# Optimization experiments

Hardware: AMD Instinct MI355X
Metric: run time of the kernel (lower is better)

Reference implementation:

```python
import jax, jax.numpy as jnp
import numpy as np

B, N, D = 1024, 7, 1024
SQRT_D = float(np.sqrt(D))
MAX_CTX, MAX_VIB = 0.24, 0.26
VIB_IDX, CTX_IDX = 3, N - 1

ADJ = jnp.asarray(np.array([
    [1, 1, 0, 0, 1, 1, 1],
    [1, 1, 1, 1, 1, 1, 1],
    [0, 1, 1, 0, 1, 0, 1],
    [0, 1, 0, 1, 1, 1, 1],
    [1, 1, 1, 1, 1, 1, 1],
    [1, 1, 0, 1, 1, 1, 1],
    [1, 1, 1, 1, 1, 1, 1]], dtype=np.float32))


def _gelu(x):
    return jax.nn.gelu(x, approximate=False)


def setup_inputs() -> dict:
    key = jax.random.key(0)
    ks = jax.random.split(key, 20)
    s = 0.02
    def w(k, shape):
        return jax.random.normal(k, shape, dtype=jnp.float32) * s
    return {
        "nodes": jax.random.normal(ks[0], (B, N, D), dtype=jnp.float32),
        "Wq": w(ks[1], (D, D)), "bq": jnp.zeros((D,), jnp.float32),
        "Wk": w(ks[2], (D, D)), "bk": jnp.zeros((D,), jnp.float32),
        "Wv": w(ks[3], (D, D)), "bv": jnp.zeros((D,), jnp.float32),
        "We1": w(ks[4], (3 * D, D)), "be1": jnp.zeros((D,), jnp.float32),
        "We2": w(ks[5], (D, 1)), "be2": jnp.zeros((1,), jnp.float32),
        "Wu1": w(ks[6], (2 * D, D)), "bu1": jnp.zeros((D,), jnp.float32),
        "Wu2": w(ks[7], (D, D)), "bu2": jnp.zeros((D,), jnp.float32),
        "Wi1": w(ks[8], (2 * D, D)), "bi1": jnp.zeros((D,), jnp.float32),
        "Wi2": w(ks[9], (D, 1)), "bi2": jnp.zeros((1,), jnp.float32),
    }


def _cap_importance(imp):
    cap = jnp.ones((N,), imp.dtype).at[VIB_IDX].set(MAX_VIB).at[CTX_IDX].set(MAX_CTX)
    free = jnp.ones((N,), imp.dtype).at[VIB_IDX].set(0.0).at[CTX_IDX].set(0.0)[None, :]
    capped = jnp.minimum(imp, cap[None, :])
    free_mass = (imp * free).sum(axis=1, keepdims=True)
    residual = jnp.clip(1.0 - capped.sum(axis=1, keepdims=True), 0.0)
    uniform = free / jnp.maximum(free.sum(axis=1, keepdims=True), 1.0)
    free_share = jnp.where(free_mass > 1e-6,
                           imp * free / jnp.maximum(free_mass, 1e-6),
                           uniform)
    redis = capped + free_share * residual
    return redis / jnp.maximum(redis.sum(axis=1, keepdims=True), 1e-6)


def _physics_loss(upd):
    norms = jnp.linalg.norm(upd, axis=-1)  # [B,N]
    dots = jnp.einsum('bnd,bmd->bnm', upd, upd)
    cos = dots / jnp.maximum(norms[:, :, None] * norms[:, None, :], 1e-8)
    eye = jnp.eye(N, dtype=upd.dtype)
    edge_loss = ((1.0 - cos) * ADJ[None]).sum() / jnp.maximum(ADJ.sum() * upd.shape[0], 1.0) * upd.shape[0]
    # note: torch sums over batch too -> divide by ADJ.sum() only
    edge_loss = ((1.0 - cos) * ADJ[None]).sum() / jnp.maximum(ADJ.sum(), 1.0)
    non_mask = (1.0 - ADJ) * (1.0 - eye)
    non_loss = (jax.nn.relu(cos - 0.35) * non_mask[None]).sum() / jnp.maximum(non_mask.sum(), 1.0)
    return edge_loss + 0.5 * non_loss


def _alignment_loss(upd, fused):
    fn = fused / jnp.maximum(jnp.linalg.norm(fused, axis=-1, keepdims=True), 1e-12)
    nn_ = upd / jnp.maximum(jnp.linalg.norm(upd, axis=-1, keepdims=True), 1e-12)
    cos = jnp.einsum('bnd,bd->bn', nn_, fn)
    return (1.0 - cos).mean()


def reference(nodes, Wq, bq, Wk, bk, Wv, bv, We1, be1, We2, be2,
              Wu1, bu1, Wu2, bu2, Wi1, bi1, Wi2, bi2):
    q = nodes @ Wq + bq
    k = nodes @ Wk + bk
    v = nodes @ Wv + bv
    logits = jnp.einsum('bnd,bmd->bnm', q, k) / SQRT_D
    # edge gate: cat([left, right, ctx]) @ We1 == left@Wa + right@Wb + ctx@Wc
    Wa, Wb, Wc = We1[:D], We1[D:2 * D], We1[2 * D:]
    la = nodes @ Wa                      # [B,N,D] (left varies over axis n)
    rb = nodes @ Wb                      # [B,N,D] (right varies over axis m)
    cc = nodes[:, -1] @ Wc               # [B,D]   (ctx broadcast)
    h = la[:, :, None, :] + rb[:, None, :, :] + cc[:, None, None, :] + be1
    edge_logits = (_gelu(h) @ We2 + be2)[..., 0]  # [B,N,N]
    masked = logits + edge_logits + (ADJ[None] - 1.0) * 10000.0
    attn = jax.nn.softmax(masked, axis=-1)
    messages = jnp.einsum('bnm,bmd->bnd', attn, v)
    upd_in = jnp.concatenate([nodes, messages], axis=-1)
    updated = _gelu(upd_in @ Wu1 + bu1) @ Wu2 + bu2 + nodes
    gq = jnp.broadcast_to(updated[:, -1:, :], updated.shape)
    imp_in = jnp.concatenate([updated, gq], axis=-1)
    imp_logits = (_gelu(imp_in @ Wi1 + bi1) @ Wi2 + bi2)[..., 0]
    imp = jax.nn.softmax(imp_logits, axis=-1)
    imp = _cap_importance(imp)
    fused = jnp.einsum('bn,bnd->bd', imp, updated)
    phys = _physics_loss(updated)
    align = _alignment_loss(updated, fused)
    return (fused, updated, imp, attn, phys + align * 0.0, align)
```

## Files before the change

kernel.cpp:

```cpp
#include <hip/hip_runtime.h>
#include <hip/hip_bf16.h>


typedef __attribute__((ext_vector_type(8))) short bf16x8;
typedef __attribute__((ext_vector_type(4))) float f32x4;

__constant__ float c_adj[49] = {
    1,1,0,0,1,1,1,
    1,1,1,1,1,1,1,
    0,1,1,0,1,0,1,
    0,1,0,1,1,1,1,
    1,1,1,1,1,1,1,
    1,1,0,1,1,1,1,
    1,1,1,1,1,1,1};

__device__ __forceinline__ float gelu_f(float x) {
    return 0.5f * x * (1.0f + erff(x * 0.7071067811865476f));
}
__device__ __forceinline__ float b2f(unsigned short u) {
    unsigned int x = ((unsigned int)u) << 16;
    union { unsigned int i; float f; } c; c.i = x; return c.f;
}
__device__ __forceinline__ unsigned short f2b(float f) {
    __hip_bfloat16 h = __float2bfloat16(f);
    union { __hip_bfloat16 b; unsigned short u; } c; c.b = h; return c.u;
}

__device__ __forceinline__ void gload_lds16(const void* g, void* l) {
    __builtin_amdgcn_global_load_lds(
        (const __attribute__((address_space(1))) unsigned int*)g,
        (__attribute__((address_space(3))) unsigned int*)l, 16, 0, 0);
}

__device__ __forceinline__ int maprow(int r, int mode) {
    if (mode == 1) return r * 7 + 6;
    if (mode == 2) return r - r % 7 + 6;
    return r;
}

__global__ __launch_bounds__(256) void gemm128(
    const unsigned short* __restrict__ A1, int a1Mode,
    const unsigned short* __restrict__ A2, int a2Mode,
    const unsigned short* __restrict__ WT, int ldw,
    const float* __restrict__ bias,
    const float* __restrict__ resid,
    float* __restrict__ Cf,
    unsigned short* __restrict__ Cb, size_t segStride,
    int K, int act)
{
    __shared__ short As[128 * 32];
    __shared__ short Bs[128 * 32];
    const int tid = threadIdx.x;
    const int lane = tid & 63;
    const int w = tid >> 6;
    const int wr = (w >> 1) * 64;
    const int wc = (w & 1) * 64;
    const int row0 = blockIdx.y * 128;
    const int col0 = blockIdx.x * 128;
    const int fr = lane & 15;
    const int fko = (((lane >> 4) ^ ((fr >> 1) & 3)) << 3);

    f32x4 acc[4][4] = {};

    for (int k0 = 0; k0 < K; k0 += 32) {
        const unsigned short* srcA; int mode; int kbase;
        if (k0 < 1024) { srcA = A1; mode = a1Mode; kbase = k0; }
        else           { srcA = A2; mode = a2Mode; kbase = k0 - 1024; }
        #pragma unroll
        for (int rnd = 0; rnd < 2; ++rnd) {
            int c = rnd * 256 + tid;
            int m = c >> 2, ch = c & 3;
            int kc = (ch ^ ((m >> 1) & 3)) * 8;
            int rr = maprow(row0 + m, mode);
            gload_lds16(srcA + (size_t)rr * 1024 + kbase + kc, &As[c * 8]);
        }
        #pragma unroll
        for (int rnd = 0; rnd < 2; ++rnd) {
            int c = rnd * 256 + tid;
            int n = c >> 2, ch = c & 3;
            int kc = (ch ^ ((n >> 1) & 3)) * 8;
            gload_lds16(WT + (size_t)(col0 + n) * ldw + k0 + kc, &Bs[c * 8]);
        }
        __syncthreads();
        bf16x8 af[4], bf_[4];
        #pragma unroll
        for (int i = 0; i < 4; ++i)
            af[i] = *(const bf16x8*)(&As[(wr + i * 16 + fr) * 32 + fko]);
        #pragma unroll
        for (int j = 0; j < 4; ++j)
            bf_[j] = *(const bf16x8*)(&Bs[(wc + j * 16 + fr) * 32 + fko]);
        #pragma unroll
        for (int i = 0; i < 4; ++i)
            #pragma unroll
            for (int j = 0; j < 4; ++j)
                acc[i][j] = __builtin_amdgcn_mfma_f32_16x16x32_bf16(
                    af[i], bf_[j], acc[i][j], 0, 0, 0);
        __syncthreads();
    }

    const int qrow = (lane >> 4) * 4;
    const int qcol = lane & 15;
    #pragma unroll
    for (int i = 0; i < 4; ++i) {
        int rbase = row0 + wr + i * 16 + qrow;
        #pragma unroll
        for (int j = 0; j < 4; ++j) {
            int c = col0 + wc + j * 16 + qcol;
            float bv = bias ? bias[c] : 0.0f;
            int seg = c >> 10, c0 = c & 1023;
            #pragma unroll
            for (int reg = 0; reg < 4; ++reg) {
                int r = rbase + reg;
                float vv = acc[i][j][reg] + bv;
                if (act) vv = gelu_f(vv);
                if (resid) vv += resid[(size_t)r * 1024 + c];
                if (Cf) Cf[(size_t)r * 1024 + c] = vv;
                if (Cb) Cb[(size_t)seg * segStride + (size_t)r * 1024 + c0] = f2b(vv);
            }
        }
    }
}

__global__ __launch_bounds__(256) void gemm64x128(
    const unsigned short* __restrict__ A1, int a1Mode,
    const unsigned short* __restrict__ A2, int a2Mode,
    const unsigned short* __restrict__ WT, int ldw,
    const float* __restrict__ bias,
    const float* __restrict__ resid,
    float* __restrict__ Cf,
    unsigned short* __restrict__ Cb,
    int K, int act)
{
    __shared__ short As[64 * 32];
    __shared__ short Bs[128 * 32];
    const int tid = threadIdx.x;
    const int lane = tid & 63;
    const int w = tid >> 6;
    const int wc = w * 32;
    const int row0 = blockIdx.y * 64;
    const int col0 = blockIdx.x * 128;
    const int fr = lane & 15;
    const int fko = (((lane >> 4) ^ ((fr >> 1) & 3)) << 3);

    f32x4 acc[4][2] = {};

    for (int k0 = 0; k0 < K; k0 += 32) {
        const unsigned short* srcA; int mode; int kbase;
        if (k0 < 1024) { srcA = A1; mode = a1Mode; kbase = k0; }
        else           { srcA = A2; mode = a2Mode; kbase = k0 - 1024; }
        {
            int m = tid >> 2, ch = tid & 3;
            int kc = (ch ^ ((m >> 1) & 3)) * 8;
            int rr = maprow(row0 + m, mode);
            gload_lds16(srcA + (size_t)rr * 1024 + kbase + kc, &As[tid * 8]);
        }
        #pragma unroll
        for (int rnd = 0; rnd < 2; ++rnd) {
            int c = rnd * 256 + tid;
            int n = c >> 2, ch = c & 3;
            int kc = (ch ^ ((n >> 1) & 3)) * 8;
            gload_lds16(WT + (size_t)(col0 + n) * ldw + k0 + kc, &Bs[c * 8]);
        }
        __syncthreads();
        bf16x8 af[4], bf_[2];
        #pragma unroll
        for (int i = 0; i < 4; ++i)
            af[i] = *(const bf16x8*)(&As[(i * 16 + fr) * 32 + fko]);
        #pragma unroll
        for (int j = 0; j < 2; ++j)
            bf_[j] = *(const bf16x8*)(&Bs[(wc + j * 16 + fr) * 32 + fko]);
        #pragma unroll
        for (int i = 0; i < 4; ++i)
            #pragma unroll
            for (int j = 0; j < 2; ++j)
                acc[i][j] = __builtin_amdgcn_mfma_f32_16x16x32_bf16(
                    af[i], bf_[j], acc[i][j], 0, 0, 0);
        __syncthreads();
    }

    const int qrow = (lane >> 4) * 4;
    const int qcol = lane & 15;
    #pragma unroll
    for (int i = 0; i < 4; ++i) {
        int rbase = row0 + i * 16 + qrow;
        #pragma unroll
        for (int j = 0; j < 2; ++j) {
            int c = col0 + wc + j * 16 + qcol;
            float bv = bias ? bias[c] : 0.0f;
            #pragma unroll
            for (int reg = 0; reg < 4; ++reg) {
                int r = rbase + reg;
                float vv = acc[i][j][reg] + bv;
                if (act) vv = gelu_f(vv);
                if (resid) vv += resid[(size_t)r * 1024 + c];
                if (Cf) Cf[(size_t)r * 1024 + c] = vv;
                if (Cb) Cb[(size_t)r * 1024 + c] = f2b(vv);
            }
        }
    }
}

__global__ __launch_bounds__(256) void cast_f2b(
    const float* __restrict__ in, unsigned short* __restrict__ out, int n)
{
    int i = (blockIdx.x * 256 + threadIdx.x) * 4;
    if (i >= n) return;
    float4 v = *(const float4*)(in + i);
    ushort4 o;
    o.x = f2b(v.x); o.y = f2b(v.y); o.z = f2b(v.z); o.w = f2b(v.w);
    *(ushort4*)(out + i) = o;
}

__global__ __launch_bounds__(256) void tcast_all(
    const float* __restrict__ Wq, const float* __restrict__ Wk,
    const float* __restrict__ Wv, const float* __restrict__ We1,
    const float* __restrict__ Wu1, const float* __restrict__ Wu2,
    const float* __restrict__ Wi1,
    unsigned short* __restrict__ WT_all, unsigned short* __restrict__ Wu1T,
    unsigned short* __restrict__ Wu2T, unsigned short* __restrict__ Wi1T)
{
    const int z = blockIdx.z;
    const float* src; unsigned short* dst; int R;
    switch (z) {
        case 0: src = Wq;            dst = WT_all;               R = 1024; break;
        case 1: src = Wk;            dst = WT_all + 1024 * 1024; R = 1024; break;
        case 2: src = Wv;            dst = WT_all + 2048 * 1024; R = 1024; break;
        case 3: src = We1;           dst = WT_all + 3072 * 1024; R = 1024; break;
        case 4: src = We1 + 1048576; dst = WT_all + 4096 * 1024; R = 1024; break;
        case 5: src = We1 + 2097152; dst = WT_all + 5120 * 1024; R = 1024; break;
        case 6: src = Wu1;           dst = Wu1T;                 R = 2048; break;
        case 7: src = Wu2;           dst = Wu2T;                 R = 1024; break;
        default: src = Wi1;          dst = Wi1T;                 R = 2048; break;
    }
    const int rt = blockIdx.y * 32;
    if (rt >= R) return;
    const int ct = blockIdx.x * 32;
    __shared__ float t[32][33];
    const int tx = threadIdx.x & 31, ty = threadIdx.x >> 5;
    #pragma unroll
    for (int s = 0; s < 4; ++s)
        t[ty + s * 8][tx] = src[(size_t)(rt + ty + s * 8) * 1024 + ct + tx];
    __syncthreads();
    #pragma unroll
    for (int s = 0; s < 4; ++s)
        dst[(size_t)(ct + ty + s * 8) * R + rt + tx] = f2b(t[tx][ty + s * 8]);
}

__global__ void build_bias(const float* __restrict__ bq,
                           const float* __restrict__ bk,
                           const float* __restrict__ bv,
                           float* __restrict__ bias_all)
{
    int i = blockIdx.x * 256 + threadIdx.x;
    if (i >= 5120) return;
    int seg = i >> 10, c = i & 1023;
    float v = 0.f;
    if (seg == 0) v = bq[c];
    else if (seg == 1) v = bk[c];
    else if (seg == 2) v = bv[c];
    bias_all[i] = v;
}

__global__ __launch_bounds__(256) void attn_msg_b(
    const unsigned short* __restrict__ q, const unsigned short* __restrict__ k,
    const unsigned short* __restrict__ v,
    const unsigned short* __restrict__ la, const unsigned short* __restrict__ rb,
    const float* __restrict__ cc,
    const float* __restrict__ We2, const float* __restrict__ be2,
    float* __restrict__ attn_out, unsigned short* __restrict__ msg)
{
    const int bn = blockIdx.x;
    const int b = bn / 7, n = bn % 7;
    const int tid = threadIdx.x;
    const int lane = tid & 63, wv = tid >> 6;
    const int d0 = tid * 4;
    __shared__ float red[8];
    __shared__ float sm[7];

    float qv[4], lav[4], ccv[4], wev[4];
    {
        ushort4 q4 = *(const ushort4*)(q + (size_t)bn * 1024 + d0);
        ushort4 l4 = *(const ushort4*)(la + (size_t)bn * 1024 + d0);
        float4 c4 = *(const float4*)(cc + (size_t)b * 1024 + d0);
        float4 w4 = *(const float4*)(We2 + d0);
        qv[0] = b2f(q4.x); qv[1] = b2f(q4.y); qv[2] = b2f(q4.z); qv[3] = b2f(q4.w);
        lav[0] = b2f(l4.x); lav[1] = b2f(l4.y); lav[2] = b2f(l4.z); lav[3] = b2f(l4.w);
        ccv[0] = c4.x; ccv[1] = c4.y; ccv[2] = c4.z; ccv[3] = c4.w;
        wev[0] = w4.x; wev[1] = w4.y; wev[2] = w4.z; wev[3] = w4.w;
    }
    for (int m = 0; m < 7; ++m) {
        ushort4 k4 = *(const ushort4*)(k  + (size_t)(b * 7 + m) * 1024 + d0);
        ushort4 r4 = *(const ushort4*)(rb + (size_t)(b * 7 + m) * 1024 + d0);
        float s1 = qv[0] * b2f(k4.x) + qv[1] * b2f(k4.y)
                 + qv[2] * b2f(k4.z) + qv[3] * b2f(k4.w);
        float s2 = gelu_f(lav[0] + b2f(r4.x) + ccv[0]) * wev[0]
                 + gelu_f(lav[1] + b2f(r4.y) + ccv[1]) * wev[1]
                 + gelu_f(lav[2] + b2f(r4.z) + ccv[2]) * wev[2]
                 + gelu_f(lav[3] + b2f(r4.w) + ccv[3]) * wev[3];
        #pragma unroll
        for (int off = 32; off > 0; off >>= 1) {
            s1 += __shfl_down(s1, off);
            s2 += __shfl_down(s2, off);
        }
        if (lane == 0) { red[wv * 2] = s1; red[wv * 2 + 1] = s2; }
        __syncthreads();
        if (tid == 0) {
            float d1 = red[0] + red[2] + red[4] + red[6];
            float d2 = red[1] + red[3] + red[5] + red[7];
            sm[m] = d1 * (1.0f / 32.0f) + d2 + be2[0]
                  + (c_adj[n * 7 + m] - 1.0f) * 10000.0f;
        }
        __syncthreads();
    }
    if (tid == 0) {
        float mx = sm[0];
        #pragma unroll
        for (int m = 1; m < 7; ++m) mx = fmaxf(mx, sm[m]);
        float e[7], s = 0.f;
        #pragma unroll
        for (int m = 0; m < 7; ++m) { e[m] = expf(sm[m] - mx); s += e[m]; }
        float inv = 1.0f / s;
        #pragma unroll
        for (int m = 0; m < 7; ++m) {
            float wgt = e[m] * inv;
            sm[m] = wgt;
            attn_out[(size_t)bn * 7 + m] = wgt;
        }
    }
    __syncthreads();
    float wr_[7];
    #pragma unroll
    for (int m = 0; m < 7; ++m) wr_[m] = sm[m];
    float s0 = 0.f, s1 = 0.f, s2 = 0.f, s3 = 0.f;
    #pragma unroll
    for (int m = 0; m < 7; ++m) {
        ushort4 v4 = *(const ushort4*)(v + (size_t)(b * 7 + m) * 1024 + d0);
        s0 += wr_[m] * b2f(v4.x); s1 += wr_[m] * b2f(v4.y);
        s2 += wr_[m] * b2f(v4.z); s3 += wr_[m] * b2f(v4.w);
    }
    ushort4 o;
    o.x = f2b(s0); o.y = f2b(s1); o.z = f2b(s2); o.w = f2b(s3);
    *(ushort4*)(msg + (size_t)bn * 1024 + d0) = o;
}

__global__ __launch_bounds__(256) void row_dot_b(
    const unsigned short* __restrict__ H, const float* __restrict__ w2,
    const float* __restrict__ b2, float* __restrict__ out)
{
    const int r = blockIdx.x;
    const int tid = threadIdx.x;
    const int lane = tid & 63, wv = tid >> 6;
    __shared__ float red[4];
    const int d0 = tid * 4;
    ushort4 h4 = *(const ushort4*)(H + (size_t)r * 1024 + d0);
    float4 w4 = *(const float4*)(w2 + d0);
    float s = b2f(h4.x) * w4.x + b2f(h4.y) * w4.y
            + b2f(h4.z) * w4.z + b2f(h4.w) * w4.w;
    #pragma unroll
    for (int off = 32; off > 0; off >>= 1) s += __shfl_down(s, off);
    if (lane == 0) red[wv] = s;
    __syncthreads();
    if (tid == 0) out[r] = red[0] + red[1] + red[2] + red[3] + b2[0];
}

__global__ __launch_bounds__(256) void imp_fused_k(
    const float* __restrict__ logits, const float* __restrict__ upd,
    float* __restrict__ imp_out, float* __restrict__ fused_out)
{
    const int b = blockIdx.x;
    const int tid = threadIdx.x;
    __shared__ float w[7];
    if (tid == 0) {
        float l[7], e[7];
        float mx = -1e30f;
        for (int i = 0; i < 7; ++i) { l[i] = logits[b * 7 + i]; mx = fmaxf(mx, l[i]); }
        float s = 0.f;
        for (int i = 0; i < 7; ++i) { e[i] = expf(l[i] - mx); s += e[i]; }
        float inv = 1.0f / s;
        float imp[7];
        for (int i = 0; i < 7; ++i) imp[i] = e[i] * inv;
        const float cap[7] = {1.f, 1.f, 1.f, 0.26f, 1.f, 1.f, 0.24f};
        const float fr[7]  = {1.f, 1.f, 1.f, 0.f,   1.f, 1.f, 0.f};
        float capped[7], capsum = 0.f, fmass = 0.f;
        for (int i = 0; i < 7; ++i) {
            capped[i] = fminf(imp[i], cap[i]);
            capsum += capped[i];
            fmass += imp[i] * fr[i];
        }
        float residual = fmaxf(1.0f - capsum, 0.0f);
        float redis[7], rs = 0.f;
        for (int i = 0; i < 7; ++i) {
            float fs = (fmass > 1e-6f) ? imp[i] * fr[i] / fmaxf(fmass, 1e-6f)
                                       : fr[i] * 0.2f;
            redis[i] = capped[i] + fs * residual;
            rs += redis[i];
        }
        float invr = 1.0f / fmaxf(rs, 1e-6f);
        for (int i = 0; i < 7; ++i) {
            float wi = redis[i] * invr;
            w[i] = wi;
            imp_out[b * 7 + i] = wi;
        }
    }
    __syncthreads();
    float wr[7];
    #pragma unroll
    for (int i = 0; i < 7; ++i) wr[i] = w[i];
    #pragma unroll
    for (int j = 0; j < 4; ++j) {
        int d = tid + j * 256;
        float s = 0.f;
        #pragma unroll
        for (int nn2 = 0; nn2 < 7; ++nn2)
            s += wr[nn2] * upd[(size_t)(b * 7 + nn2) * 1024 + d];
        fused_out[(size_t)b * 1024 + d] = s;
    }
}

__global__ void zero_acc(float* a) { if (threadIdx.x < 4) a[threadIdx.x] = 0.f; }

__global__ __launch_bounds__(256) void physics_k(
    const float* __restrict__ upd, const float* __restrict__ fused,
    float* __restrict__ accums)
{
    const int b = blockIdx.x;
    const int tid = threadIdx.x;
    const int lane = tid & 63, wv = tid >> 6;
    __shared__ float u[7][1024];
    __shared__ float f[1024];
    __shared__ float wred[4][36];
    for (int idx = tid; idx < 7 * 1024; idx += 256)
        u[idx >> 10][idx & 1023] = upd[(size_t)b * 7168 + idx];
    for (int d = tid; d < 1024; d += 256)
        f[d] = fused[(size_t)b * 1024 + d];
    __syncthreads();

    float vals[36];
    #pragma unroll
    for (int i = 0; i < 36; ++i) vals[i] = 0.f;
    for (int d = tid; d < 1024; d += 256) {
        float x[7];
        #pragma unroll
        for (int n = 0; n < 7; ++n) x[n] = u[n][d];
        float fv = f[d];
        int idx = 0;
        #pragma unroll
        for (int n = 0; n < 7; ++n) {
            #pragma unroll
            for (int m = n; m < 7; ++m) vals[idx++] += x[n] * x[m];
        }
        #pragma unroll
        for (int n = 0; n < 7; ++n) vals[28 + n] += x[n] * fv;
        vals[35] += fv * fv;
    }
    #pragma unroll
    for (int i = 0; i < 36; ++i) {
        float s = vals[i];
        #pragma unroll
        for (int off = 32; off > 0; off >>= 1) s += __shfl_down(s, off);
        if (lane == 0) wred[wv][i] = s;
    }
    __syncthreads();
    if (tid == 0) {
        float tv[36];
        for (int i = 0; i < 36; ++i)
            tv[i] = wred[0][i] + wred[1][i] + wred[2][i] + wred[3][i];
        auto didx = [](int n, int m) -> int {
            if (n > m) { int t = n; n = m; m = t; }
            return n * 7 - n * (n - 1) / 2 + (m - n);
        };
        float norms[7];
        for (int n = 0; n < 7; ++n) norms[n] = sqrtf(tv[didx(n, n)]);
        float e = 0.f, nl = 0.f;
        for (int n = 0; n < 7; ++n)
            for (int m = 0; m < 7; ++m) {
                float cos_ = tv[didx(n, m)] / fmaxf(norms[n] * norms[m], 1e-8f);
                float adj = c_adj[n * 7 + m];
                e += (1.0f - cos_) * adj;
                if (adj == 0.0f && n != m) nl += fmaxf(cos_ - 0.35f, 0.0f);
            }
        float fnorm = sqrtf(tv[35]);
        float al = 0.f;
        for (int n = 0; n < 7; ++n) {
            float cosn = tv[28 + n] /
                         (fmaxf(norms[n], 1e-12f) * fmaxf(fnorm, 1e-12f));
            al += 1.0f - cosn;
        }
        atomicAdd(&accums[0], e);
        atomicAdd(&accums[1], nl);
        atomicAdd(&accums[2], al);
    }
}

__global__ void finalize_k(const float* __restrict__ a,
                           float* __restrict__ phys_o,
                           float* __restrict__ align_o)
{
    phys_o[0]  = a[0] / 41.0f + 0.5f * (a[1] / 8.0f);
    align_o[0] = a[2] * (1.0f / 7168.0f);
}

extern "C" void kernel_launch(void* const* d_in, const int* in_sizes, int n_in,
                              void* d_out, int out_size, void* d_ws, size_t ws_size,
                              hipStream_t stream)
{
    const float* nodes = (const float*)d_in[0];
    const float* Wq  = (const float*)d_in[1];
    const float* bq  = (const float*)d_in[2];
    const float* Wk  = (const float*)d_in[3];
    const float* bk  = (const float*)d_in[4];
    const float* Wv  = (const float*)d_in[5];
    const float* bv  = (const float*)d_in[6];
    const float* We1 = (const float*)d_in[7];
    const float* be1 = (const float*)d_in[8];
    const float* We2 = (const float*)d_in[9];
    const float* be2 = (const float*)d_in[10];
    const float* Wu1 = (const float*)d_in[11];
    const float* bu1 = (const float*)d_in[12];
    const float* Wu2 = (const float*)d_in[13];
    const float* bu2 = (const float*)d_in[14];
    const float* Wi1 = (const float*)d_in[15];
    const float* bi1 = (const float*)d_in[16];
    const float* Wi2 = (const float*)d_in[17];
    const float* bi2 = (const float*)d_in[18];

    float* out = (float*)d_out;
    float* fused_o = out;
    float* upd_o   = out + 1048576;
    float* imp_o   = out + 1048576 + 7340032;
    float* attn_o  = imp_o + 7168;
    float* phys_o  = attn_o + 50176;
    float* align_o = phys_o + 1;

    const size_t BIG = 7340032;
    const size_t MEG = 1048576;
    char* p = (char*)d_ws;
    unsigned short* nodes_b = (unsigned short*)p; p += BIG * 2;
    unsigned short* qb      = (unsigned short*)p; p += BIG * 2;
    unsigned short* kb      = (unsigned short*)p; p += BIG * 2;
    unsigned short* vb      = (unsigned short*)p; p += BIG * 2;
    unsigned short* lab     = (unsigned short*)p; p += BIG * 2;
    unsigned short* rbb     = (unsigned short*)p; p += BIG * 2;
    unsigned short* WT_all  = (unsigned short*)p; p += (size_t)6144 * 1024 * 2;
    unsigned short* Wu1T    = (unsigned short*)p; p += 2 * MEG * 2;
    unsigned short* Wu2T    = (unsigned short*)p; p += MEG * 2;
    unsigned short* Wi1T    = (unsigned short*)p; p += 2 * MEG * 2;
    float* bias_all = (float*)p; p += 5120 * 4;
    float* ccf = (float*)p; p += MEG * 4;
    float* il  = (float*)p; p += 7168 * 4;
    float* acc = (float*)p; p += 4 * 4;
    unsigned short* msgb = lab;
    unsigned short* hub  = qb;
    unsigned short* updb = kb;
    unsigned short* hib  = vb;

    dim3 blk(256);

    cast_f2b<<<dim3(7168), blk, 0, stream>>>(nodes, nodes_b, 7340032);
    tcast_all<<<dim3(32, 64, 9), blk, 0, stream>>>(Wq, Wk, Wv, We1, Wu1, Wu2, Wi1,
                                                   WT_all, Wu1T, Wu2T, Wi1T);
    build_bias<<<dim3(20), blk, 0, stream>>>(bq, bk, bv, bias_all);

    gemm128<<<dim3(40, 56), blk, 0, stream>>>(
        nodes_b, 0, nullptr, 0, WT_all, 1024, bias_all, nullptr,
        nullptr, qb, BIG, 1024, 0);

    gemm64x128<<<dim3(8, 16), blk, 0, stream>>>(
        nodes_b, 1, nullptr, 0, WT_all + (size_t)5120 * 1024, 1024, be1, nullptr,
        ccf, nullptr, 1024, 0);

    attn_msg_b<<<dim3(7168), blk, 0, stream>>>(qb, kb, vb, lab, rbb, ccf, We2, be2,
                                               attn_o, msgb);

    gemm128<<<dim3(8, 56), blk, 0, stream>>>(
        nodes_b, 0, msgb, 0, Wu1T, 2048, bu1, nullptr, nullptr, hub, 0, 2048, 1);
    gemm128<<<dim3(8, 56), blk, 0, stream>>>(
        hub, 0, nullptr, 0, Wu2T, 1024, bu2, nodes, upd_o, updb, 0, 1024, 0);
    gemm128<<<dim3(8, 56), blk, 0, stream>>>(
        updb, 0, updb, 2, Wi1T, 2048, bi1, nullptr, nullptr, hib, 0, 2048, 1);

    row_dot_b<<<dim3(7168), blk, 0, stream>>>(hib, Wi2, bi2, il);
    imp_fused_k<<<dim3(1024), blk, 0, stream>>>(il, upd_o, imp_o, fused_o);
    zero_acc<<<1, 64, 0, stream>>>(acc);
    physics_k<<<dim3(1024), blk, 0, stream>>>(upd_o, fused_o, acc);
    finalize_k<<<1, 1, 0, stream>>>(acc, phys_o, align_o);
}
```

Before: 579.1 us.

## Replace fused QKV/edge projection GEMM with 256x256 tiled, 4-stage pipelined kernel

Adds a 512-thread GEMM kernel with 256x256 output tiles, a 4-deep LDS ring buffer fed by direct global-to-LDS loads, XOR-swizzled LDS layout, XCD-aware block remapping and split half-tile MFMA phases with priority hints. It replaces the 128x128 GEMM for the large 7168x5120 projection. The goal is more data reuse per tile and better overlap of loads with MFMA work. The cost is 128 KB of LDS and fewer, larger workgroups (560), which limits occupancy.

Result: slower. 591.8 us (+2.2%).

```diff
diff --git a/kernel.cpp b/kernel.cpp
--- a/kernel.cpp
+++ b/kernel.cpp
@@ -36,6 +36,145 @@
     if (mode == 1) return r * 7 + 6;
     if (mode == 2) return r - r % 7 + 6;
     return r;
+}
+
+__global__ __launch_bounds__(512) void gemm256(
+    const unsigned short* __restrict__ A,
+    const unsigned short* __restrict__ WT, int ldw,
+    const float* __restrict__ bias,
+    unsigned short* __restrict__ Cb, size_t segStride,
+    int K)
+{
+    __shared__ short As[4 * 256 * 32];
+    __shared__ short Bs[4 * 256 * 32];
+
+    const int tid  = threadIdx.x;
+    const int lane = tid & 63;
+    const int w    = tid >> 6;
+    const int wm   = w >> 2;
+    const int wn   = w & 3;
+    const int wmr  = wm * 128;
+    const int wnr  = wn * 64;
+
+    int lin = blockIdx.y * gridDim.x + blockIdx.x;
+    const int nwg = gridDim.x * gridDim.y;
+    const int cpx = nwg >> 3;
+    lin = (lin & 7) * cpx + (lin >> 3);
+    const int row0 = (lin / gridDim.x) * 256;
+    const int col0 = (lin % gridDim.x) * 256;
+
+    const int fr  = lane & 15;
+    const int fko = (((lane >> 4) ^ ((fr >> 1) & 3)) << 3);
+
+    int srow[2], skc[2], ldsoff[2];
+    #pragma unroll
+    for (int ld = 0; ld < 2; ++ld) {
+        int s = ld * 512 + tid;
+        int r = s >> 2, ch = s & 3;
+        srow[ld]   = r;
+        skc[ld]    = (ch ^ ((r >> 1) & 3)) * 8;
+        ldsoff[ld] = s * 8;
+    }
+
+    const int NT = K >> 5;
+
+    f32x4 acc[8][4] = {};
+    bf16x8 af[4], bf_[4];
+
+    #pragma unroll
+    for (int u0 = 0; u0 < 4; ++u0) {
+        int tu = u0 >> 1, slot = tu;
+        #pragma unroll
+        for (int ld = 0; ld < 2; ++ld) {
+            if ((u0 & 1) == 0)
+                gload_lds16(A + (size_t)(row0 + srow[ld]) * K + tu * 32 + skc[ld],
+                            &As[slot * 8192 + ldsoff[ld]]);
+            else
+                gload_lds16(WT + (size_t)(col0 + srow[ld]) * ldw + tu * 32 + skc[ld],
+                            &Bs[slot * 8192 + ldsoff[ld]]);
+        }
+    }
+    asm volatile("s_waitcnt vmcnt(4)" ::: "memory");
+    asm volatile("s_barrier" ::: "memory");
+
+    for (int kt = 0; kt < NT; ++kt) {
+        const short* Ab = &As[(kt & 3) * 8192];
+        const short* Bb = &Bs[(kt & 3) * 8192];
+
+        {
+            #pragma unroll
+            for (int i = 0; i < 4; ++i)
+                af[i] = *(const bf16x8*)(Ab + (wmr + i * 16 + fr) * 32 + fko);
+            #pragma unroll
+            for (int j = 0; j < 4; ++j)
+                bf_[j] = *(const bf16x8*)(Bb + (wnr + j * 16 + fr) * 32 + fko);
+            int u = 2 * kt + 4;
+            if (u < 2 * NT) {
+                int tu = u >> 1, slot = tu & 3;
+                #pragma unroll
+                for (int ld = 0; ld < 2; ++ld)
+                    gload_lds16(A + (size_t)(row0 + srow[ld]) * K + tu * 32 + skc[ld],
+                                &As[slot * 8192 + ldsoff[ld]]);
+            }
+            asm volatile("s_barrier" ::: "memory");
+            asm volatile("s_waitcnt lgkmcnt(0)" ::: "memory");
+            __builtin_amdgcn_s_setprio(1);
+            #pragma unroll
+            for (int i = 0; i < 4; ++i)
+                #pragma unroll
+                for (int j = 0; j < 4; ++j)
+                    acc[i][j] = __builtin_amdgcn_mfma_f32_16x16x32_bf16(
+                        af[i], bf_[j], acc[i][j], 0, 0, 0);
+            __builtin_amdgcn_s_setprio(0);
+            asm volatile("s_barrier" ::: "memory");
+        }
+
+        {
+            #pragma unroll
+            for (int i = 0; i < 4; ++i)
+                af[i] = *(const bf16x8*)(Ab + (wmr + (4 + i) * 16 + fr) * 32 + fko);
+            int u = 2 * kt + 5;
+            if (u < 2 * NT) {
+                int tu = u >> 1, slot = tu & 3;
+                #pragma unroll
+                for (int ld = 0; ld < 2; ++ld)
+                    gload_lds16(WT + (size_t)(col0 + srow[ld]) * ldw + tu * 32 + skc[ld],
+                                &Bs[slot * 8192 + ldsoff[ld]]);
+            }
+            if (kt >= NT - 2) asm volatile("s_waitcnt vmcnt(0)" ::: "memory");
+            else              asm volatile("s_waitcnt vmcnt(4)" ::: "memory");
+            asm volatile("s_barrier" ::: "memory");
+            asm volatile("s_waitcnt lgkmcnt(0)" ::: "memory");
+            __builtin_amdgcn_s_setprio(1);
+            #pragma unroll
+            for (int i = 0; i < 4; ++i)
+                #pragma unroll
+                for (int j = 0; j < 4; ++j)
+                    acc[4 + i][j] = __builtin_amdgcn_mfma_f32_16x16x32_bf16(
+                        af[i], bf_[j], acc[4 + i][j], 0, 0, 0);
+            __builtin_amdgcn_s_setprio(0);
+            asm volatile("s_barrier" ::: "memory");
+        }
+    }
+
+    const int qrow = (lane >> 4) * 4;
+    const int qcol = lane & 15;
+    #pragma unroll
+    for (int mf = 0; mf < 8; ++mf) {
+        int rbase = row0 + wmr + mf * 16 + qrow;
+        #pragma unroll
+        for (int nf = 0; nf < 4; ++nf) {
+            int c = col0 + wnr + nf * 16 + qcol;
+            float bv = bias ? bias[c] : 0.0f;
+            int seg = c >> 10, c0 = c & 1023;
+            #pragma unroll
+            for (int reg = 0; reg < 4; ++reg) {
+                int r = rbase + reg;
+                Cb[(size_t)seg * segStride + (size_t)r * 1024 + c0] =
+                    f2b(acc[mf][nf][reg] + bv);
+            }
+        }
+    }
 }
 
 __global__ __launch_bounds__(256) void gemm128(
@@ -561,9 +700,8 @@
                                                    WT_all, Wu1T, Wu2T, Wi1T);
     build_bias<<<dim3(20), blk, 0, stream>>>(bq, bk, bv, bias_all);
 
-    gemm128<<<dim3(40, 56), blk, 0, stream>>>(
-        nodes_b, 0, nullptr, 0, WT_all, 1024, bias_all, nullptr,
-        nullptr, qb, BIG, 1024, 0);
+    gemm256<<<dim3(20, 28), dim3(512), 0, stream>>>(
+        nodes_b, WT_all, 1024, bias_all, qb, BIG, 1024);
 
     gemm64x128<<<dim3(8, 16), blk, 0, stream>>>(
         nodes_b, 1, nullptr, 0, WT_all + (size_t)5120 * 1024, 1024, be1, nullptr,
```

## Double-buffer LDS in gemm128 with XCD-aware block remap and fold zero kernel

Applied to the files above, without the earlier changes.

The main GEMM now uses two LDS buffers so the next K-tile's global-to-LDS loads are issued before the MFMAs on the current tile, with one waitcnt and barrier per iteration instead of two syncthreads. Workgroup IDs are remapped so consecutive tiles land on the same XCD, which should improve L2 reuse, and MFMA sections run at raised wave priority. The separate zero_acc launch is folded into build_bias. The cost is doubled LDS use, which may lower occupancy, and the remap assumes the grid size divides evenly by 8.

After: 581.4 us. Within noise of the previous version (+0.4%).

```diff
diff --git a/kernel.cpp b/kernel.cpp
--- a/kernel.cpp
+++ b/kernel.cpp
@@ -38,7 +38,7 @@
     return r;
 }
 
-__global__ __launch_bounds__(256) void gemm128(
+__global__ __launch_bounds__(256) void gemm128db(
     const unsigned short* __restrict__ A1, int a1Mode,
     const unsigned short* __restrict__ A2, int a2Mode,
     const unsigned short* __restrict__ WT, int ldw,
@@ -48,54 +48,81 @@
     unsigned short* __restrict__ Cb, size_t segStride,
     int K, int act)
 {
-    __shared__ short As[128 * 32];
-    __shared__ short Bs[128 * 32];
+    __shared__ short As[2][128 * 32];
+    __shared__ short Bs[2][128 * 32];
     const int tid = threadIdx.x;
     const int lane = tid & 63;
     const int w = tid >> 6;
     const int wr = (w >> 1) * 64;
     const int wc = (w & 1) * 64;
-    const int row0 = blockIdx.y * 128;
-    const int col0 = blockIdx.x * 128;
+
+    int lin = blockIdx.y * gridDim.x + blockIdx.x;
+    const int nwg = gridDim.x * gridDim.y;
+    const int cpx = nwg >> 3;
+    lin = (lin & 7) * cpx + (lin >> 3);
+    const int row0 = (lin / gridDim.x) * 128;
+    const int col0 = (lin % gridDim.x) * 128;
+
     const int fr = lane & 15;
     const int fko = (((lane >> 4) ^ ((fr >> 1) & 3)) << 3);
 
-    f32x4 acc[4][4] = {};
-
-    for (int k0 = 0; k0 < K; k0 += 32) {
+    const int NTt = K >> 5;
+
+    auto stage = [&](int ktn) {
+        int k0n = ktn * 32;
         const unsigned short* srcA; int mode; int kbase;
-        if (k0 < 1024) { srcA = A1; mode = a1Mode; kbase = k0; }
-        else           { srcA = A2; mode = a2Mode; kbase = k0 - 1024; }
+        if (k0n < 1024) { srcA = A1; mode = a1Mode; kbase = k0n; }
+        else            { srcA = A2; mode = a2Mode; kbase = k0n - 1024; }
+        short* Adst = &As[ktn & 1][0];
+        short* Bdst = &Bs[ktn & 1][0];
         #pragma unroll
         for (int rnd = 0; rnd < 2; ++rnd) {
             int c = rnd * 256 + tid;
             int m = c >> 2, ch = c & 3;
             int kc = (ch ^ ((m >> 1) & 3)) * 8;
             int rr = maprow(row0 + m, mode);
-            gload_lds16(srcA + (size_t)rr * 1024 + kbase + kc, &As[c * 8]);
+            gload_lds16(srcA + (size_t)rr * 1024 + kbase + kc, Adst + c * 8);
         }
         #pragma unroll
         for (int rnd = 0; rnd < 2; ++rnd) {
             int c = rnd * 256 + tid;
             int n = c >> 2, ch = c & 3;
             int kc = (ch ^ ((n >> 1) & 3)) * 8;
-            gload_lds16(WT + (size_t)(col0 + n) * ldw + k0 + kc, &Bs[c * 8]);
-        }
-        __syncthreads();
-        bf16x8 af[4], bf_[4];
+            gload_lds16(WT + (size_t)(col0 + n) * ldw + k0n + kc, Bdst + c * 8);
+        }
+    };
+
+    f32x4 acc[4][4] = {};
+
+    stage(0);
+    asm volatile("s_waitcnt vmcnt(0)" ::: "memory");
+    asm volatile("s_barrier" ::: "memory");
+
+    for (int kt = 0; kt < NTt; ++kt) {
+        const short* Ab = &As[kt & 1][0];
+        const short* Bb = &Bs[kt & 1][0];
+
+        if (kt + 1 < NTt) stage(kt + 1);
+
+        bf16x8 af[4], bfv[4];
         #pragma unroll
         for (int i = 0; i < 4; ++i)
-            af[i] = *(const bf16x8*)(&As[(wr + i * 16 + fr) * 32 + fko]);
+            af[i] = *(const bf16x8*)(Ab + (wr + i * 16 + fr) * 32 + fko);
         #pragma unroll
         for (int j = 0; j < 4; ++j)
-            bf_[j] = *(const bf16x8*)(&Bs[(wc + j * 16 + fr) * 32 + fko]);
+            bfv[j] = *(const bf16x8*)(Bb + (wc + j * 16 + fr) * 32 + fko);
+
+        __builtin_amdgcn_s_setprio(1);
         #pragma unroll
         for (int i = 0; i < 4; ++i)
             #pragma unroll
             for (int j = 0; j < 4; ++j)
                 acc[i][j] = __builtin_amdgcn_mfma_f32_16x16x32_bf16(
-                    af[i], bf_[j], acc[i][j], 0, 0, 0);
-        __syncthreads();
+                    af[i], bfv[j], acc[i][j], 0, 0, 0);
+        __builtin_amdgcn_s_setprio(0);
+
+        asm volatile("s_waitcnt vmcnt(0)" ::: "memory");
+        asm volatile("s_barrier" ::: "memory");
     }
 
     const int qrow = (lane >> 4) * 4;
@@ -249,9 +276,11 @@
 __global__ void build_bias(const float* __restrict__ bq,
                            const float* __restrict__ bk,
                            const float* __restrict__ bv,
-                           float* __restrict__ bias_all)
+                           float* __restrict__ bias_all,
+                           float* __restrict__ acc)
 {
     int i = blockIdx.x * 256 + threadIdx.x;
+    if (i < 4) acc[i] = 0.f;
     if (i >= 5120) return;
     int seg = i >> 10, c = i & 1023;
     float v = 0.f;
@@ -416,8 +445,6 @@
         fused_out[(size_t)b * 1024 + d] = s;
     }
 }
-
-__global__ void zero_acc(float* a) { if (threadIdx.x < 4) a[threadIdx.x] = 0.f; }
 
 __global__ __launch_bounds__(256) void physics_k(
     const float* __restrict__ upd, const float* __restrict__ fused,
@@ -559,9 +586,9 @@
     cast_f2b<<<dim3(7168), blk, 0, stream>>>(nodes, nodes_b, 7340032);
     tcast_all<<<dim3(32, 64, 9), blk, 0, stream>>>(Wq, Wk, Wv, We1, Wu1, Wu2, Wi1,
                                                    WT_all, Wu1T, Wu2T, Wi1T);
-    build_bias<<<dim3(20), blk, 0, stream>>>(bq, bk, bv, bias_all);
-
-    gemm128<<<dim3(40, 56), blk, 0, stream>>>(
+    build_bias<<<dim3(20), blk, 0, stream>>>(bq, bk, bv, bias_all, acc);
+
+    gemm128db<<<dim3(40, 56), blk, 0, stream>>>(
         nodes_b, 0, nullptr, 0, WT_all, 1024, bias_all, nullptr,
         nullptr, qb, BIG, 1024, 0);
 
@@ -572,16 +599,15 @@
     attn_msg_b<<<dim3(7168), blk, 0, stream>>>(qb, kb, vb, lab, rbb, ccf, We2, be2,
                                                attn_o, msgb);
 
-    gemm128<<<dim3(8, 56), blk, 0, stream>>>(
+    gemm128db<<<dim3(8, 56), blk, 0, stream>>>(
         nodes_b, 0, msgb, 0, Wu1T, 2048, bu1, nullptr, nullptr, hub, 0, 2048, 1);
-    gemm128<<<dim3(8, 56), blk, 0, stream>>>(
+    gemm128db<<<dim3(8, 56), blk, 0, stream>>>(
         hub, 0, nullptr, 0, Wu2T, 1024, bu2, nodes, upd_o, updb, 0, 1024, 0);
-    gemm128<<<dim3(8, 56), blk, 0, stream>>>(
+    gemm128db<<<dim3(8, 56), blk, 0, stream>>>(
         updb, 0, updb, 2, Wi1T, 2048, bi1, nullptr, nullptr, hib, 0, 2048, 1);
 
     row_dot_b<<<dim3(7168), blk, 0, stream>>>(hib, Wi2, bi2, il);
     imp_fused_k<<<dim3(1024), blk, 0, stream>>>(il, upd_o, imp_o, fused_o);
-    zero_acc<<<1, 64, 0, stream>>>(acc);
     physics_k<<<dim3(1024), blk, 0, stream>>>(upd_o, fused_o, acc);
     finalize_k<<<1, 1, 0, stream>>>(acc, phys_o, align_o);
 }
```
